# Kernel optimization log

Measured on AMD Instinct MI355X. Metric: run time of the kernel, lower is better.

## Reference

```python
import jax, jax.numpy as jnp
import numpy as np

OBS, ACT, D, S, H = 64, 8, 256, 32, 256  # obs_dim, act_dim, deter_dim, stoch_dim, hidden_dim
B, T = 1024, 128


def setup_inputs() -> dict:
    key = jax.random.key(0)
    ks = jax.random.split(key, 24)
    rn = lambda k, shape, s=0.05: jax.random.normal(k, shape, jnp.float32) * s
    return {
        'obs_seq': jax.random.normal(ks[0], (B, T, OBS), jnp.float32),
        'act_seq': jax.random.normal(ks[1], (B, T, ACT), jnp.float32),
        'noise':   jax.random.normal(ks[2], (T, B, S), jnp.float32),
        # obs encoder (two Linear+ELU layers)
        'W_e1': rn(ks[3], (H, OBS)), 'b_e1': rn(ks[4], (H,)),
        'W_e2': rn(ks[5], (H, H)),   'b_e2': rn(ks[6], (H,)),
        # GRU (PyTorch gate order: reset, update, new)
        'W_ih': rn(ks[7], (3 * D, S + ACT)), 'W_hh': rn(ks[8], (3 * D, D)),
        'b_ih': jnp.zeros((3 * D,), jnp.float32), 'b_hh': jnp.zeros((3 * D,), jnp.float32),
        # prior net: deter -> hidden -> 2*stoch
        'W_p1': rn(ks[9], (H, D)),  'b_p1': rn(ks[10], (H,)),
        'W_p2': rn(ks[11], (2 * S, H)), 'b_p2': rn(ks[12], (2 * S,)),
        # post net: deter+hidden -> hidden -> 2*stoch
        'W_q1': rn(ks[13], (H, D + H)), 'b_q1': rn(ks[14], (H,)),
        'W_q2': rn(ks[15], (2 * S, H)), 'b_q2': rn(ks[16], (2 * S,)),
    }


def _stats(stats):
    mean, logstd = jnp.split(stats, 2, axis=-1)
    return mean, jnp.exp(jnp.clip(logstd, -7.0, 5.0))


def reference(obs_seq, act_seq, noise, W_e1, b_e1, W_e2, b_e2,
              W_ih, W_hh, b_ih, b_hh, W_p1, b_p1, W_p2, b_p2,
              W_q1, b_q1, W_q2, b_q2):
    elu = jax.nn.elu
    Bsz = obs_seq.shape[0]
    obs_T = jnp.transpose(obs_seq, (1, 0, 2))  # [T,B,OBS]
    act_T = jnp.transpose(act_seq, (1, 0, 2))  # [T,B,ACT]

    def step(h, xs):
        o, a, eps = xs
        # prior from current deterministic state
        pm, ps = _stats(elu(h @ W_p1.T + b_p1) @ W_p2.T + b_p2)
        # obs embedding (hidden-dim output of obs_encoder)
        emb = elu(elu(o @ W_e1.T + b_e1) @ W_e2.T + b_e2)
        # posterior from (h, obs embedding)
        qm, qs = _stats(elu(jnp.concatenate([h, emb], -1) @ W_q1.T + b_q1) @ W_q2.T + b_q2)
        z = qm + qs * eps  # reparameterized sample
        # GRU cell step (torch semantics)
        x = jnp.concatenate([z, a], -1)
        gi = x @ W_ih.T + b_ih
        gh = h @ W_hh.T + b_hh
        gi_r, gi_z, gi_n = jnp.split(gi, 3, -1)
        gh_r, gh_z, gh_n = jnp.split(gh, 3, -1)
        r = jax.nn.sigmoid(gi_r + gh_r)
        u = jax.nn.sigmoid(gi_z + gh_z)
        n = jnp.tanh(gi_n + r * gh_n)
        h_new = (1.0 - u) * n + u * h
        out_t = jnp.concatenate([h, z, pm, ps, qm, qs], -1)  # [B, D+5S]
        return h_new, out_t

    h0 = jnp.zeros((Bsz, D), obs_seq.dtype)
    _, ys = jax.lax.scan(step, h0, (obs_T, act_T, noise))
    return jnp.transpose(ys, (1, 0, 2))  # [B, T, D+5S] = cat(h, z, prior_mean, prior_std, post_mean, post_std)
```

## Files before the change

### kernel.cpp

```cpp
#include <hip/hip_runtime.h>
#include <hip/hip_bf16.h>
#include <string.h>

#define TT 128
#define BB 1024
#define DD 256
#define SS 32
#define HHID 256
#define NC 1280
#define RR 4

typedef __attribute__((ext_vector_type(8))) short bf16x8;
typedef __attribute__((ext_vector_type(4))) float f32x4;

__device__ __forceinline__ float eluf(float x)   { return x > 0.f ? x : __expf(x) - 1.f; }
__device__ __forceinline__ float sigf(float x)   { return 1.f / (1.f + __expf(-x)); }
__device__ __forceinline__ float tanhf_(float x) { float e = __expf(2.f * x); return (e - 1.f) / (e + 1.f); }
__device__ __forceinline__ float clip75(float x) { return fminf(fmaxf(x, -7.f), 5.f); }

__device__ __forceinline__ void bar_lds() {
    asm volatile("s_waitcnt lgkmcnt(0)\n\ts_barrier" ::: "memory");
}

__device__ __forceinline__ float2 bf2f2(unsigned int u) {
    union { unsigned int i; float f; } a, b;
    a.i = (u & 0xffffu) << 16;
    b.i = u & 0xffff0000u;
    return make_float2(a.f, b.f);
}

__global__ void transpose_k(const float* __restrict__ src, float* __restrict__ dst,
                            int N, int K, int soff, int sld, int dld, int dcoff)
{
    int idx = blockIdx.x * 256 + threadIdx.x;
    if (idx >= N * K) return;
    int k = idx / N, n = idx - k * N;
    dst[k * dld + dcoff + n] = src[n * sld + soff + k];
}

__global__ void prep_wcomb(const float* __restrict__ Wp1, const float* __restrict__ Wq1,
                           const float* __restrict__ Whh, __hip_bfloat16* __restrict__ dst)
{
    int idx = blockIdx.x * 256 + threadIdx.x;
    if (idx >= NC * DD) return;
    int j = idx & 7, lane = (idx >> 3) & 63, ks = (idx >> 9) & 7, nt = idx >> 12;
    int n = nt * 16 + (lane & 15);
    int k = ks * 32 + (lane >> 4) * 8 + j;
    float v;
    if (n < 256)      v = Wp1[n * 256 + k];
    else if (n < 512) v = Wq1[(n - 256) * 512 + k];
    else              v = Whh[(n - 512) * 256 + k];
    dst[idx] = __float2bfloat16(v);
}

__global__ void prep_w2(const float* __restrict__ W, __hip_bfloat16* __restrict__ dst)
{
    int idx = blockIdx.x * 256 + threadIdx.x;
    if (idx >= 64 * 256) return;
    int par = idx & 1, q = (idx >> 1) & 3, l = (idx >> 3) & 63, kg = idx >> 9;
    dst[idx] = __float2bfloat16(W[l * 256 + kg * 8 + q * 2 + par]);
}

__global__ void prep_wih(const float* __restrict__ W, __hip_bfloat16* __restrict__ dst)
{
    int idx = blockIdx.x * 256 + threadIdx.x;
    if (idx >= 20 * 256 * 8) return;
    int par = idx & 1, g = (idx >> 1) & 3, j = (idx >> 3) & 255, kp = idx >> 11;
    float v = 0.f;
    if (g < 3) v = W[(g * 256 + j) * 40 + kp * 2 + par];
    dst[idx] = __float2bfloat16(v);
}

__global__ void __launch_bounds__(256) obs_enc_k(
    const float* __restrict__ obs, const float* __restrict__ We1t,
    const float* __restrict__ be1, const float* __restrict__ We2t,
    const float* __restrict__ be2, const float* __restrict__ Wq1et,
    const float* __restrict__ bq1, float* __restrict__ Qpre)
{
    __shared__ float buf0[32 * 256];
    __shared__ float buf1[32 * 256];
    const int tid = threadIdx.x;
    const int r0 = blockIdx.x * 32;
    const int tx = tid & 31, ty = tid >> 5;
    const int colb = tx * 8;
    float acc[4][8];

#pragma unroll
    for (int i = 0; i < 4; ++i)
#pragma unroll
        for (int j = 0; j < 8; ++j) acc[i][j] = 0.f;
#pragma unroll 4
    for (int k = 0; k < 64; ++k) {
        float4 w0 = *(const float4*)&We1t[k * 256 + colb];
        float4 w1 = *(const float4*)&We1t[k * 256 + colb + 4];
#pragma unroll
        for (int i = 0; i < 4; ++i) {
            float a = obs[(r0 + ty * 4 + i) * 64 + k];
            acc[i][0] += a * w0.x; acc[i][1] += a * w0.y; acc[i][2] += a * w0.z; acc[i][3] += a * w0.w;
            acc[i][4] += a * w1.x; acc[i][5] += a * w1.y; acc[i][6] += a * w1.z; acc[i][7] += a * w1.w;
        }
    }
#pragma unroll
    for (int i = 0; i < 4; ++i)
#pragma unroll
        for (int j = 0; j < 8; ++j)
            buf0[(ty * 4 + i) * 256 + colb + j] = eluf(acc[i][j] + be1[colb + j]);
    __syncthreads();

#pragma unroll
    for (int i = 0; i < 4; ++i)
#pragma unroll
        for (int j = 0; j < 8; ++j) acc[i][j] = 0.f;
#pragma unroll 4
    for (int k = 0; k < 256; ++k) {
        float4 w0 = *(const float4*)&We2t[k * 256 + colb];
        float4 w1 = *(const float4*)&We2t[k * 256 + colb + 4];
#pragma unroll
        for (int i = 0; i < 4; ++i) {
            float a = buf0[(ty * 4 + i) * 256 + k];
            acc[i][0] += a * w0.x; acc[i][1] += a * w0.y; acc[i][2] += a * w0.z; acc[i][3] += a * w0.w;
            acc[i][4] += a * w1.x; acc[i][5] += a * w1.y; acc[i][6] += a * w1.z; acc[i][7] += a * w1.w;
        }
    }
#pragma unroll
    for (int i = 0; i < 4; ++i)
#pragma unroll
        for (int j = 0; j < 8; ++j)
            buf1[(ty * 4 + i) * 256 + colb + j] = eluf(acc[i][j] + be2[colb + j]);
    __syncthreads();

#pragma unroll
    for (int i = 0; i < 4; ++i)
#pragma unroll
        for (int j = 0; j < 8; ++j) acc[i][j] = 0.f;
#pragma unroll 4
    for (int k = 0; k < 256; ++k) {
        float4 w0 = *(const float4*)&Wq1et[k * 256 + colb];
        float4 w1 = *(const float4*)&Wq1et[k * 256 + colb + 4];
#pragma unroll
        for (int i = 0; i < 4; ++i) {
            float a = buf1[(ty * 4 + i) * 256 + k];
            acc[i][0] += a * w0.x; acc[i][1] += a * w0.y; acc[i][2] += a * w0.z; acc[i][3] += a * w0.w;
            acc[i][4] += a * w1.x; acc[i][5] += a * w1.y; acc[i][6] += a * w1.z; acc[i][7] += a * w1.w;
        }
    }
#pragma unroll
    for (int i = 0; i < 4; ++i) {
        int r = r0 + ty * 4 + i;
        int b = r >> 7, t = r & (TT - 1);
        float* dst = Qpre + ((size_t)t * BB + b) * HHID + colb;
#pragma unroll
        for (int j = 0; j < 8; ++j)
            dst[j] = acc[i][j] + bq1[colb + j];
    }
}

__global__ void __launch_bounds__(512, 2) rssm_seq(
    const float* __restrict__ act, const float* __restrict__ noise,
    const __hip_bfloat16* __restrict__ Wfrag, const float* __restrict__ b_p1,
    const float* __restrict__ b_hh, const float* __restrict__ Qpre,
    const uint4* __restrict__ Wp2q, const float* __restrict__ b_p2,
    const uint4* __restrict__ Wq2q, const float* __restrict__ b_q2,
    const uint4* __restrict__ Wihq, const float* __restrict__ b_ih,
    float* __restrict__ out)
{
    __shared__ float CA[RR][NC];
    __shared__ float h32[RR][DD];
    __shared__ __hip_bfloat16 hbf[16][264];
    __shared__ float zl[RR][SS];
    __shared__ float actl[RR][8];
    __shared__ float qbuf[2][RR][HHID];

    const int tid = threadIdx.x;
    const int wave = tid >> 6, lane = tid & 63;
    const int blk = blockIdx.x;

    for (int i = tid; i < 16 * 264; i += 512) ((unsigned short*)hbf)[i] = 0;
    for (int i = tid; i < RR * DD; i += 512) ((float*)h32)[i] = 0.f;
    {
        const int qi = tid * 2, qreg = qi >> 8, qcol = qi & 255;
        *(float2*)&qbuf[0][qreg][qcol] =
            *(const float2*)&Qpre[((size_t)0 * BB + blk * RR + qreg) * HHID + qcol];
    }
    __syncthreads();

    const int am = lane & 15, aq = lane >> 4;
    const bf16x8* wp = (const bf16x8*)Wfrag + (size_t)wave * 80 * 64 + lane;

    for (int t = 0; t < TT; ++t) {
        if (tid < RR * 8) {
            int row = tid >> 3, c = tid & 7;
            actl[row][c] = act[((size_t)(blk * RR + row) * TT + t) * 8 + c];
        }
        float nval = 0.f;
        if (wave >= 4 && lane < 32)
            nval = noise[((size_t)t * BB + blk * RR + (wave & 3)) * SS + lane];
        float2 qv = make_float2(0.f, 0.f);
        if (t + 1 < TT) {
            const int qi = tid * 2, qreg = qi >> 8, qcol = qi & 255;
            qv = *(const float2*)&Qpre[((size_t)(t + 1) * BB + blk * RR + qreg) * HHID + qcol];
        }

        bf16x8 afr[8];
#pragma unroll
        for (int ks = 0; ks < 8; ++ks)
            afr[ks] = *(const bf16x8*)&hbf[am][ks * 32 + aq * 8];

        bf16x8 bbuf[2][8];
#pragma unroll
        for (int ks = 0; ks < 8; ++ks) bbuf[0][ks] = wp[(size_t)ks * 64];
#pragma unroll 2
        for (int i = 0; i < 10; ++i) {
            const int cb = i & 1;
            if (i < 9) {
#pragma unroll
                for (int ks = 0; ks < 8; ++ks)
                    bbuf[cb ^ 1][ks] = wp[(size_t)((i + 1) * 8 + ks) * 64];
            }
            f32x4 acc = {0.f, 0.f, 0.f, 0.f};
#pragma unroll
            for (int ks = 0; ks < 8; ++ks)
                acc = __builtin_amdgcn_mfma_f32_16x16x32_bf16(afr[ks], bbuf[cb][ks], acc, 0, 0, 0);
            const int nt = wave * 10 + i;
            if (lane < 16) {
                const int col = nt * 16 + lane;
                if (nt < 16) {
#pragma unroll
                    for (int reg = 0; reg < RR; ++reg)
                        CA[reg][col] = eluf(acc[reg] + b_p1[col]);
                } else if (nt < 32) {
#pragma unroll
                    for (int reg = 0; reg < RR; ++reg)
                        CA[reg][col] = eluf(acc[reg] + qbuf[t & 1][reg][col - 256]);
                } else {
#pragma unroll
                    for (int reg = 0; reg < RR; ++reg)
                        CA[reg][col] = acc[reg] + b_hh[col - 512];
                }
            }
        }
        bar_lds();

        {
            const int row = wave & 3, isq = wave >> 2;
            const float* car = CA[row] + (isq ? 256 : 0);
            const uint4* W2 = isq ? Wq2q : Wp2q;
            float dA = isq ? b_q2[lane] : b_p2[lane];
            float dB = 0.f;
#pragma unroll 4
            for (int kg = 0; kg < 32; ++kg) {
                uint4 wv = W2[kg * 64 + lane];
                float4 c0 = *(const float4*)&car[kg * 8];
                float4 c1 = *(const float4*)&car[kg * 8 + 4];
                float2 w;
                w = bf2f2(wv.x); dA += c0.x * w.x + c0.y * w.y;
                w = bf2f2(wv.y); dB += c0.z * w.x + c0.w * w.y;
                w = bf2f2(wv.z); dA += c1.x * w.x + c1.y * w.y;
                w = bf2f2(wv.w); dB += c1.z * w.x + c1.w * w.y;
            }
            float d = dA + dB;
            const int r = blk * RR + row;
            float* orow = out + ((size_t)r * TT + t) * 416;
            float v = (lane < 32) ? d : __expf(clip75(d));
            if (!isq) {
                orow[288 + lane] = v;
            } else {
                orow[352 + lane] = v;
                float qs_hi = __shfl(v, lane + 32, 64);
                if (lane < 32) {
                    float z = v + qs_hi * nval;
                    zl[row][lane] = z;
                    orow[256 + lane] = z;
                }
            }
        }
        if (t + 1 < TT) {
            const int qi = tid * 2;
            *(float2*)&qbuf[(t + 1) & 1][qi >> 8][qi & 255] = qv;
        }
        bar_lds();

        {
            const int j = tid & 255, rh = tid >> 8;
            float g0[2], g1[2], g2[2];
            float br = b_ih[j], bz = b_ih[256 + j], bn = b_ih[512 + j];
#pragma unroll
            for (int rr = 0; rr < 2; ++rr) { g0[rr] = br; g1[rr] = bz; g2[rr] = bn; }
#pragma unroll 4
            for (int kp = 0; kp < 20; ++kp) {
                uint4 w4 = Wihq[kp * 256 + j];
                float2 wr = bf2f2(w4.x), wz = bf2f2(w4.y), wn = bf2f2(w4.z);
#pragma unroll
                for (int rr = 0; rr < 2; ++rr) {
                    const int r = rh * 2 + rr;
                    float2 a2 = (kp < 16) ? *(const float2*)&zl[r][kp * 2]
                                          : *(const float2*)&actl[r][(kp - 16) * 2];
                    g0[rr] += a2.x * wr.x + a2.y * wr.y;
                    g1[rr] += a2.x * wz.x + a2.y * wz.y;
                    g2[rr] += a2.x * wn.x + a2.y * wn.y;
                }
            }
#pragma unroll
            for (int rr = 0; rr < 2; ++rr) {
                const int r = rh * 2 + rr;
                float rg = sigf(g0[rr] + CA[r][512 + j]);
                float ug = sigf(g1[rr] + CA[r][768 + j]);
                float ng = tanhf_(g2[rr] + rg * CA[r][1024 + j]);
                float hold = h32[r][j];
                float hn = (1.f - ug) * ng + ug * hold;
                out[((size_t)(blk * RR + r) * TT + t) * 416 + j] = hold;
                h32[r][j] = hn;
                hbf[r][j] = __float2bfloat16(hn);
            }
        }
        bar_lds();
    }
}

extern "C" void kernel_launch(void* const* d_in, const int* in_sizes, int n_in,
                              void* d_out, int out_size, void* d_ws, size_t ws_size,
                              hipStream_t stream)
{
    const float* obs   = (const float*)d_in[0];
    const float* act   = (const float*)d_in[1];
    const float* noise = (const float*)d_in[2];
    const float* W_e1  = (const float*)d_in[3];
    const float* b_e1  = (const float*)d_in[4];
    const float* W_e2  = (const float*)d_in[5];
    const float* b_e2  = (const float*)d_in[6];
    const float* W_ih  = (const float*)d_in[7];
    const float* W_hh  = (const float*)d_in[8];
    const float* b_ih  = (const float*)d_in[9];
    const float* b_hh  = (const float*)d_in[10];
    const float* W_p1  = (const float*)d_in[11];
    const float* b_p1  = (const float*)d_in[12];
    const float* W_p2  = (const float*)d_in[13];
    const float* b_p2  = (const float*)d_in[14];
    const float* W_q1  = (const float*)d_in[15];
    const float* b_q1  = (const float*)d_in[16];
    const float* W_q2  = (const float*)d_in[17];
    const float* b_q2  = (const float*)d_in[18];
    float* outp = (float*)d_out;

    const size_t qpre_elems = (size_t)TT * BB * HHID;
    float* Qpre  = (float*)d_ws;
    float* We1t  = Qpre + qpre_elems;
    float* We2t  = We1t + 64 * 256;
    float* Wq1et = We2t + 256 * 256;
    __hip_bfloat16* Wfrag = (__hip_bfloat16*)(Wq1et + 256 * 256);
    __hip_bfloat16* Wp2b  = Wfrag + NC * DD;
    __hip_bfloat16* Wq2b  = Wp2b + 64 * 256;
    __hip_bfloat16* Wihb  = Wq2b + 64 * 256;
    size_t total_bytes = (char*)(Wihb + 20 * 256 * 8) - (char*)d_ws;
    if (ws_size < total_bytes) return;

    auto tl = [&](const float* s, float* d, int N, int K, int soff, int sld, int dld, int dcoff) {
        int tot = N * K;
        transpose_k<<<(tot + 255) / 256, 256, 0, stream>>>(s, d, N, K, soff, sld, dld, dcoff);
    };
    tl(W_e1, We1t, 256, 64, 0, 64, 256, 0);
    tl(W_e2, We2t, 256, 256, 0, 256, 256, 0);
    tl(W_q1, Wq1et, 256, 256, 256, 512, 256, 0);

    prep_wcomb<<<(NC * DD + 255) / 256, 256, 0, stream>>>(W_p1, W_q1, W_hh, Wfrag);
    prep_w2<<<(64 * 256 + 255) / 256, 256, 0, stream>>>(W_p2, Wp2b);
    prep_w2<<<(64 * 256 + 255) / 256, 256, 0, stream>>>(W_q2, Wq2b);
    prep_wih<<<(20 * 256 * 8 + 255) / 256, 256, 0, stream>>>(W_ih, Wihb);

    obs_enc_k<<<dim3((BB * TT) / 32), dim3(256), 0, stream>>>(
        obs, We1t, b_e1, We2t, b_e2, Wq1et, b_q1, Qpre);

    rssm_seq<<<dim3(BB / RR), dim3(512), 0, stream>>>(
        act, noise, Wfrag, b_p1, b_hh, Qpre,
        (const uint4*)Wp2b, b_p2,
        (const uint4*)Wq2b, b_q2,
        (const uint4*)Wihb, b_ih, outp);
}
```

Before: 2.307 ms.

## Double recurrent kernel block to 1024 threads, halving per-wave MFMA tiles

The sequential RSSM kernel now launches 1024 threads (16 waves) per block instead of 512. Each wave computes 5 of the 80 combined-weight column tiles instead of 10, and each thread in the GRU phase handles one batch row instead of two. The aim is to shorten the per-timestep critical path by spreading work across more waves. In exchange, waves 8-15 sit idle in the prior/posterior phase, barriers span more waves, and the 1024-thread bound may cap registers per thread or lower how many blocks can be resident per CU.

```diff
diff --git a/kernel.cpp b/kernel.cpp
--- a/kernel.cpp
+++ b/kernel.cpp
@@ -155,7 +155,7 @@
     }
 }
 
-__global__ void __launch_bounds__(512, 2) rssm_seq(
+__global__ void __launch_bounds__(1024) rssm_seq(
     const float* __restrict__ act, const float* __restrict__ noise,
     const __hip_bfloat16* __restrict__ Wfrag, const float* __restrict__ b_p1,
     const float* __restrict__ b_hh, const float* __restrict__ Qpre,
@@ -175,9 +175,9 @@
     const int wave = tid >> 6, lane = tid & 63;
     const int blk = blockIdx.x;
 
-    for (int i = tid; i < 16 * 264; i += 512) ((unsigned short*)hbf)[i] = 0;
-    for (int i = tid; i < RR * DD; i += 512) ((float*)h32)[i] = 0.f;
-    {
+    for (int i = tid; i < 16 * 264; i += 1024) ((unsigned short*)hbf)[i] = 0;
+    for (int i = tid; i < RR * DD; i += 1024) ((float*)h32)[i] = 0.f;
+    if (tid < 512) {
         const int qi = tid * 2, qreg = qi >> 8, qcol = qi & 255;
         *(float2*)&qbuf[0][qreg][qcol] =
             *(const float2*)&Qpre[((size_t)0 * BB + blk * RR + qreg) * HHID + qcol];
@@ -185,7 +185,7 @@
     __syncthreads();
 
     const int am = lane & 15, aq = lane >> 4;
-    const bf16x8* wp = (const bf16x8*)Wfrag + (size_t)wave * 80 * 64 + lane;
+    const bf16x8* wp = (const bf16x8*)Wfrag + (size_t)wave * 40 * 64 + lane;
 
     for (int t = 0; t < TT; ++t) {
         if (tid < RR * 8) {
@@ -193,10 +193,10 @@
             actl[row][c] = act[((size_t)(blk * RR + row) * TT + t) * 8 + c];
         }
         float nval = 0.f;
-        if (wave >= 4 && lane < 32)
+        if (wave >= 4 && wave < 8 && lane < 32)
             nval = noise[((size_t)t * BB + blk * RR + (wave & 3)) * SS + lane];
         float2 qv = make_float2(0.f, 0.f);
-        if (t + 1 < TT) {
+        if (t + 1 < TT && tid < 512) {
             const int qi = tid * 2, qreg = qi >> 8, qcol = qi & 255;
             qv = *(const float2*)&Qpre[((size_t)(t + 1) * BB + blk * RR + qreg) * HHID + qcol];
         }
@@ -210,9 +210,9 @@
 #pragma unroll
         for (int ks = 0; ks < 8; ++ks) bbuf[0][ks] = wp[(size_t)ks * 64];
 #pragma unroll 2
-        for (int i = 0; i < 10; ++i) {
+        for (int i = 0; i < 5; ++i) {
             const int cb = i & 1;
-            if (i < 9) {
+            if (i < 4) {
 #pragma unroll
                 for (int ks = 0; ks < 8; ++ks)
                     bbuf[cb ^ 1][ks] = wp[(size_t)((i + 1) * 8 + ks) * 64];
@@ -221,7 +221,7 @@
 #pragma unroll
             for (int ks = 0; ks < 8; ++ks)
                 acc = __builtin_amdgcn_mfma_f32_16x16x32_bf16(afr[ks], bbuf[cb][ks], acc, 0, 0, 0);
-            const int nt = wave * 10 + i;
+            const int nt = wave * 5 + i;
             if (lane < 16) {
                 const int col = nt * 16 + lane;
                 if (nt < 16) {
@@ -241,7 +241,7 @@
         }
         bar_lds();
 
-        {
+        if (wave < 8) {
             const int row = wave & 3, isq = wave >> 2;
             const float* car = CA[row] + (isq ? 256 : 0);
             const uint4* W2 = isq ? Wq2q : Wp2q;
@@ -274,44 +274,33 @@
                 }
             }
         }
-        if (t + 1 < TT) {
+        if (t + 1 < TT && tid < 512) {
             const int qi = tid * 2;
             *(float2*)&qbuf[(t + 1) & 1][qi >> 8][qi & 255] = qv;
         }
         bar_lds();
 
         {
-            const int j = tid & 255, rh = tid >> 8;
-            float g0[2], g1[2], g2[2];
-            float br = b_ih[j], bz = b_ih[256 + j], bn = b_ih[512 + j];
-#pragma unroll
-            for (int rr = 0; rr < 2; ++rr) { g0[rr] = br; g1[rr] = bz; g2[rr] = bn; }
+            const int j = tid & 255, r = tid >> 8;
+            float g0 = b_ih[j], g1 = b_ih[256 + j], g2 = b_ih[512 + j];
 #pragma unroll 4
             for (int kp = 0; kp < 20; ++kp) {
                 uint4 w4 = Wihq[kp * 256 + j];
                 float2 wr = bf2f2(w4.x), wz = bf2f2(w4.y), wn = bf2f2(w4.z);
-#pragma unroll
-                for (int rr = 0; rr < 2; ++rr) {
-                    const int r = rh * 2 + rr;
-                    float2 a2 = (kp < 16) ? *(const float2*)&zl[r][kp * 2]
-                                          : *(const float2*)&actl[r][(kp - 16) * 2];
-                    g0[rr] += a2.x * wr.x + a2.y * wr.y;
-                    g1[rr] += a2.x * wz.x + a2.y * wz.y;
-                    g2[rr] += a2.x * wn.x + a2.y * wn.y;
-                }
-            }
-#pragma unroll
-            for (int rr = 0; rr < 2; ++rr) {
-                const int r = rh * 2 + rr;
-                float rg = sigf(g0[rr] + CA[r][512 + j]);
-                float ug = sigf(g1[rr] + CA[r][768 + j]);
-                float ng = tanhf_(g2[rr] + rg * CA[r][1024 + j]);
-                float hold = h32[r][j];
-                float hn = (1.f - ug) * ng + ug * hold;
-                out[((size_t)(blk * RR + r) * TT + t) * 416 + j] = hold;
-                h32[r][j] = hn;
-                hbf[r][j] = __float2bfloat16(hn);
-            }
+                float2 a2 = (kp < 16) ? *(const float2*)&zl[r][kp * 2]
+                                      : *(const float2*)&actl[r][(kp - 16) * 2];
+                g0 += a2.x * wr.x + a2.y * wr.y;
+                g1 += a2.x * wz.x + a2.y * wz.y;
+                g2 += a2.x * wn.x + a2.y * wn.y;
+            }
+            float rg = sigf(g0 + CA[r][512 + j]);
+            float ug = sigf(g1 + CA[r][768 + j]);
+            float ng = tanhf_(g2 + rg * CA[r][1024 + j]);
+            float hold = h32[r][j];
+            float hn = (1.f - ug) * ng + ug * hold;
+            out[((size_t)(blk * RR + r) * TT + t) * 416 + j] = hold;
+            h32[r][j] = hn;
+            hbf[r][j] = __float2bfloat16(hn);
         }
         bar_lds();
     }
@@ -370,7 +359,7 @@
     obs_enc_k<<<dim3((BB * TT) / 32), dim3(256), 0, stream>>>(
         obs, We1t, b_e1, We2t, b_e2, Wq1et, b_q1, Qpre);
 
-    rssm_seq<<<dim3(BB / RR), dim3(512), 0, stream>>>(
+    rssm_seq<<<dim3(BB / RR), dim3(1024), 0, stream>>>(
         act, noise, Wfrag, b_p1, b_hh, Qpre,
         (const uint4*)Wp2b, b_p2,
         (const uint4*)Wq2b, b_q2,
```

New measurement: 4.939 ms. 2.14x slower.

## Rewrite observation encoder with bf16 MFMA and pre-fragmented weights

Applied to the files above, without the earlier changes.

Replaces the scalar fp32 FMA obs encoder (three chained 256-wide linear layers over all B*T rows) with a bf16 MFMA 16x16x32 version. Weights are pre-packed into per-lane fragment layout by a new prep kernel, and intermediate activations are stored in LDS as bf16. Each block now handles 64 rows. This cuts the large parallel encoder's compute cost, at the price of reduced precision in the embedding path.

```diff
diff --git a/kernel.cpp b/kernel.cpp
--- a/kernel.cpp
+++ b/kernel.cpp
@@ -29,13 +29,14 @@
     return make_float2(a.f, b.f);
 }
 
-__global__ void transpose_k(const float* __restrict__ src, float* __restrict__ dst,
-                            int N, int K, int soff, int sld, int dld, int dcoff)
-{
-    int idx = blockIdx.x * 256 + threadIdx.x;
-    if (idx >= N * K) return;
-    int k = idx / N, n = idx - k * N;
-    dst[k * dld + dcoff + n] = src[n * sld + soff + k];
+__device__ __forceinline__ bf16x8 pack8(const float* p) {
+    bf16x8 r;
+#pragma unroll
+    for (int j = 0; j < 8; ++j) {
+        __hip_bfloat16 h = __float2bfloat16(p[j]);
+        r[j] = *reinterpret_cast<short*>(&h);
+    }
+    return r;
 }
 
 __global__ void prep_wcomb(const float* __restrict__ Wp1, const float* __restrict__ Wq1,
@@ -53,6 +54,20 @@
     dst[idx] = __float2bfloat16(v);
 }
 
+__global__ void prep_bfrag(const float* __restrict__ src, __hip_bfloat16* __restrict__ dst,
+                           int N, int K, int soff, int sld)
+{
+    int idx = blockIdx.x * 256 + threadIdx.x;
+    if (idx >= N * K) return;
+    int j = idx & 7, lane = (idx >> 3) & 63;
+    int t = idx >> 9;
+    int ksn = K >> 5;
+    int ks = t % ksn, nt = t / ksn;
+    int n = nt * 16 + (lane & 15);
+    int k = ks * 32 + (lane >> 4) * 8 + j;
+    dst[idx] = __float2bfloat16(src[n * sld + soff + k]);
+}
+
 __global__ void prep_w2(const float* __restrict__ W, __hip_bfloat16* __restrict__ dst)
 {
     int idx = blockIdx.x * 256 + threadIdx.x;
@@ -72,86 +87,90 @@
 }
 
 __global__ void __launch_bounds__(256) obs_enc_k(
-    const float* __restrict__ obs, const float* __restrict__ We1t,
-    const float* __restrict__ be1, const float* __restrict__ We2t,
-    const float* __restrict__ be2, const float* __restrict__ Wq1et,
-    const float* __restrict__ bq1, float* __restrict__ Qpre)
-{
-    __shared__ float buf0[32 * 256];
-    __shared__ float buf1[32 * 256];
+    const float* __restrict__ obs,
+    const bf16x8* __restrict__ Wf1, const float* __restrict__ be1,
+    const bf16x8* __restrict__ Wf2, const float* __restrict__ be2,
+    const bf16x8* __restrict__ Wf3, const float* __restrict__ bq1,
+    float* __restrict__ Qpre)
+{
+    __shared__ __hip_bfloat16 H1[64][264];
+    __shared__ __hip_bfloat16 H2[64][264];
     const int tid = threadIdx.x;
-    const int r0 = blockIdx.x * 32;
-    const int tx = tid & 31, ty = tid >> 5;
-    const int colb = tx * 8;
-    float acc[4][8];
-
-#pragma unroll
-    for (int i = 0; i < 4; ++i)
-#pragma unroll
-        for (int j = 0; j < 8; ++j) acc[i][j] = 0.f;
-#pragma unroll 4
-    for (int k = 0; k < 64; ++k) {
-        float4 w0 = *(const float4*)&We1t[k * 256 + colb];
-        float4 w1 = *(const float4*)&We1t[k * 256 + colb + 4];
-#pragma unroll
-        for (int i = 0; i < 4; ++i) {
-            float a = obs[(r0 + ty * 4 + i) * 64 + k];
-            acc[i][0] += a * w0.x; acc[i][1] += a * w0.y; acc[i][2] += a * w0.z; acc[i][3] += a * w0.w;
-            acc[i][4] += a * w1.x; acc[i][5] += a * w1.y; acc[i][6] += a * w1.z; acc[i][7] += a * w1.w;
-        }
-    }
-#pragma unroll
-    for (int i = 0; i < 4; ++i)
-#pragma unroll
-        for (int j = 0; j < 8; ++j)
-            buf0[(ty * 4 + i) * 256 + colb + j] = eluf(acc[i][j] + be1[colb + j]);
+    const int wave = tid >> 6, lane = tid & 63;
+    const int am = lane & 15, aq = lane >> 4;
+    const int r0 = blockIdx.x * 64;
+    const int arow = wave * 16 + am;
+    const int orow = wave * 16 + aq * 4;
+
+    bf16x8 af0, af1;
+    {
+        float tmp[8];
+        const float* src = obs + (size_t)(r0 + arow) * 64 + aq * 8;
+        *(float4*)&tmp[0] = *(const float4*)&src[0];
+        *(float4*)&tmp[4] = *(const float4*)&src[4];
+        af0 = pack8(tmp);
+        *(float4*)&tmp[0] = *(const float4*)&src[32];
+        *(float4*)&tmp[4] = *(const float4*)&src[36];
+        af1 = pack8(tmp);
+    }
+    {
+        const bf16x8* w1 = Wf1 + lane;
+#pragma unroll 2
+        for (int nt = 0; nt < 16; ++nt) {
+            f32x4 acc = {0.f, 0.f, 0.f, 0.f};
+            acc = __builtin_amdgcn_mfma_f32_16x16x32_bf16(af0, w1[(size_t)(nt * 2 + 0) * 64], acc, 0, 0, 0);
+            acc = __builtin_amdgcn_mfma_f32_16x16x32_bf16(af1, w1[(size_t)(nt * 2 + 1) * 64], acc, 0, 0, 0);
+            const int col = nt * 16 + am;
+            float b = be1[col];
+#pragma unroll
+            for (int reg = 0; reg < 4; ++reg)
+                H1[orow + reg][col] = __float2bfloat16(eluf(acc[reg] + b));
+        }
+    }
     __syncthreads();
 
-#pragma unroll
-    for (int i = 0; i < 4; ++i)
-#pragma unroll
-        for (int j = 0; j < 8; ++j) acc[i][j] = 0.f;
-#pragma unroll 4
-    for (int k = 0; k < 256; ++k) {
-        float4 w0 = *(const float4*)&We2t[k * 256 + colb];
-        float4 w1 = *(const float4*)&We2t[k * 256 + colb + 4];
-#pragma unroll
-        for (int i = 0; i < 4; ++i) {
-            float a = buf0[(ty * 4 + i) * 256 + k];
-            acc[i][0] += a * w0.x; acc[i][1] += a * w0.y; acc[i][2] += a * w0.z; acc[i][3] += a * w0.w;
-            acc[i][4] += a * w1.x; acc[i][5] += a * w1.y; acc[i][6] += a * w1.z; acc[i][7] += a * w1.w;
-        }
-    }
-#pragma unroll
-    for (int i = 0; i < 4; ++i)
-#pragma unroll
-        for (int j = 0; j < 8; ++j)
-            buf1[(ty * 4 + i) * 256 + colb + j] = eluf(acc[i][j] + be2[colb + j]);
+    {
+        bf16x8 af[8];
+#pragma unroll
+        for (int ks = 0; ks < 8; ++ks)
+            af[ks] = *(const bf16x8*)&H1[arow][ks * 32 + aq * 8];
+        const bf16x8* w2 = Wf2 + lane;
+#pragma unroll 2
+        for (int nt = 0; nt < 16; ++nt) {
+            f32x4 acc = {0.f, 0.f, 0.f, 0.f};
+#pragma unroll
+            for (int ks = 0; ks < 8; ++ks)
+                acc = __builtin_amdgcn_mfma_f32_16x16x32_bf16(af[ks], w2[(size_t)(nt * 8 + ks) * 64], acc, 0, 0, 0);
+            const int col = nt * 16 + am;
+            float b = be2[col];
+#pragma unroll
+            for (int reg = 0; reg < 4; ++reg)
+                H2[orow + reg][col] = __float2bfloat16(eluf(acc[reg] + b));
+        }
+    }
     __syncthreads();
 
-#pragma unroll
-    for (int i = 0; i < 4; ++i)
-#pragma unroll
-        for (int j = 0; j < 8; ++j) acc[i][j] = 0.f;
-#pragma unroll 4
-    for (int k = 0; k < 256; ++k) {
-        float4 w0 = *(const float4*)&Wq1et[k * 256 + colb];
-        float4 w1 = *(const float4*)&Wq1et[k * 256 + colb + 4];
-#pragma unroll
-        for (int i = 0; i < 4; ++i) {
-            float a = buf1[(ty * 4 + i) * 256 + k];
-            acc[i][0] += a * w0.x; acc[i][1] += a * w0.y; acc[i][2] += a * w0.z; acc[i][3] += a * w0.w;
-            acc[i][4] += a * w1.x; acc[i][5] += a * w1.y; acc[i][6] += a * w1.z; acc[i][7] += a * w1.w;
-        }
-    }
-#pragma unroll
-    for (int i = 0; i < 4; ++i) {
-        int r = r0 + ty * 4 + i;
-        int b = r >> 7, t = r & (TT - 1);
-        float* dst = Qpre + ((size_t)t * BB + b) * HHID + colb;
-#pragma unroll
-        for (int j = 0; j < 8; ++j)
-            dst[j] = acc[i][j] + bq1[colb + j];
+    {
+        bf16x8 af[8];
+#pragma unroll
+        for (int ks = 0; ks < 8; ++ks)
+            af[ks] = *(const bf16x8*)&H2[arow][ks * 32 + aq * 8];
+        const bf16x8* w3 = Wf3 + lane;
+#pragma unroll 2
+        for (int nt = 0; nt < 16; ++nt) {
+            f32x4 acc = {0.f, 0.f, 0.f, 0.f};
+#pragma unroll
+            for (int ks = 0; ks < 8; ++ks)
+                acc = __builtin_amdgcn_mfma_f32_16x16x32_bf16(af[ks], w3[(size_t)(nt * 8 + ks) * 64], acc, 0, 0, 0);
+            const int col = nt * 16 + am;
+            float b = bq1[col];
+#pragma unroll
+            for (int reg = 0; reg < 4; ++reg) {
+                const int r = r0 + orow + reg;
+                const int bb = r >> 7, tt = r & (TT - 1);
+                Qpre[((size_t)tt * BB + bb) * HHID + col] = acc[reg] + b;
+            }
+        }
     }
 }
 
@@ -344,31 +363,27 @@
 
     const size_t qpre_elems = (size_t)TT * BB * HHID;
     float* Qpre  = (float*)d_ws;
-    float* We1t  = Qpre + qpre_elems;
-    float* We2t  = We1t + 64 * 256;
-    float* Wq1et = We2t + 256 * 256;
-    __hip_bfloat16* Wfrag = (__hip_bfloat16*)(Wq1et + 256 * 256);
+    __hip_bfloat16* Wfrag = (__hip_bfloat16*)(Qpre + qpre_elems);
     __hip_bfloat16* Wp2b  = Wfrag + NC * DD;
     __hip_bfloat16* Wq2b  = Wp2b + 64 * 256;
     __hip_bfloat16* Wihb  = Wq2b + 64 * 256;
-    size_t total_bytes = (char*)(Wihb + 20 * 256 * 8) - (char*)d_ws;
+    __hip_bfloat16* We1f  = Wihb + 20 * 256 * 8;
+    __hip_bfloat16* We2f  = We1f + 256 * 64;
+    __hip_bfloat16* Wq1f  = We2f + 256 * 256;
+    size_t total_bytes = (char*)(Wq1f + 256 * 256) - (char*)d_ws;
     if (ws_size < total_bytes) return;
-
-    auto tl = [&](const float* s, float* d, int N, int K, int soff, int sld, int dld, int dcoff) {
-        int tot = N * K;
-        transpose_k<<<(tot + 255) / 256, 256, 0, stream>>>(s, d, N, K, soff, sld, dld, dcoff);
-    };
-    tl(W_e1, We1t, 256, 64, 0, 64, 256, 0);
-    tl(W_e2, We2t, 256, 256, 0, 256, 256, 0);
-    tl(W_q1, Wq1et, 256, 256, 256, 512, 256, 0);
 
     prep_wcomb<<<(NC * DD + 255) / 256, 256, 0, stream>>>(W_p1, W_q1, W_hh, Wfrag);
     prep_w2<<<(64 * 256 + 255) / 256, 256, 0, stream>>>(W_p2, Wp2b);
     prep_w2<<<(64 * 256 + 255) / 256, 256, 0, stream>>>(W_q2, Wq2b);
     prep_wih<<<(20 * 256 * 8 + 255) / 256, 256, 0, stream>>>(W_ih, Wihb);
-
-    obs_enc_k<<<dim3((BB * TT) / 32), dim3(256), 0, stream>>>(
-        obs, We1t, b_e1, We2t, b_e2, Wq1et, b_q1, Qpre);
+    prep_bfrag<<<(256 * 64 + 255) / 256, 256, 0, stream>>>(W_e1, We1f, 256, 64, 0, 64);
+    prep_bfrag<<<(256 * 256 + 255) / 256, 256, 0, stream>>>(W_e2, We2f, 256, 256, 0, 256);
+    prep_bfrag<<<(256 * 256 + 255) / 256, 256, 0, stream>>>(W_q1, Wq1f, 256, 256, 256, 512);
+
+    obs_enc_k<<<dim3((BB * TT) / 64), dim3(256), 0, stream>>>(
+        obs, (const bf16x8*)We1f, b_e1, (const bf16x8*)We2f, b_e2,
+        (const bf16x8*)Wq1f, b_q1, Qpre);
 
     rssm_seq<<<dim3(BB / RR), dim3(512), 0, stream>>>(
         act, noise, Wfrag, b_p1, b_hh, Qpre,
```

Result: faster. 1.879 ms (-18.6%).
